# Performance work log

Measured on AMD Instinct MI355X. Metric: run time of the kernel, lower is better.

The kernel has to match this reference:

```python
import jax, jax.numpy as jnp
import numpy as np
import math

B, L, D, H = 2, 2048, 1024, 16
DK = D // H

def setup_inputs() -> dict:
    key = jax.random.key(0)
    ks = jax.random.split(key, 12)
    s = 1.0 / math.sqrt(D)
    inp = {
        "Q": jax.random.normal(ks[0], (B, L, D), jnp.float32),
        "K": jax.random.normal(ks[1], (B, L, D), jnp.float32),
        "V": jax.random.normal(ks[2], (B, L, D), jnp.float32),
        "mask": jnp.tril(jnp.ones((L, L), jnp.bool_))[None, None],  # [1,1,L,L] causal
        "Wq_w": jax.random.normal(ks[3], (D, D), jnp.float32) * s,
        "Wq_b": jnp.zeros((D,), jnp.float32),
        "Wk_w": jax.random.normal(ks[4], (D, D), jnp.float32) * s,
        "Wk_b": jnp.zeros((D,), jnp.float32),
        "Wv_w": jax.random.normal(ks[5], (D, D), jnp.float32) * s,
        "Wv_b": jnp.zeros((D,), jnp.float32),
        "fc_w": jax.random.normal(ks[6], (D, D), jnp.float32) * s,
        "fc_b": jnp.zeros((D,), jnp.float32),
    }
    return inp

def reference(Q, K, V, mask, Wq_w, Wq_b, Wk_w, Wk_b, Wv_w, Wv_b, fc_w, fc_b):
    # torch Linear: y = x @ W.T + b
    def split_heads(x):
        return x.reshape(B, L, H, DK).transpose(0, 2, 1, 3)  # [B,H,L,DK]
    q = split_heads(Q @ Wq_w.T + Wq_b)
    k = split_heads(K @ Wk_w.T + Wk_b)
    v = split_heads(V @ Wv_w.T + Wv_b)
    scores = jnp.einsum("bhqd,bhkd->bhqk", q, k) / math.sqrt(DK)
    scores = jnp.where(mask, scores, jnp.float32(-1e9))
    attn = jax.nn.softmax(scores, axis=-1)
    out = jnp.einsum("bhqk,bhkd->bhqd", attn, v)
    out = out.transpose(0, 2, 1, 3).reshape(B, L, D)
    return out @ fc_w.T + fc_b
```

## Files before the change

kernel.cpp:

```cpp
#include <hip/hip_runtime.h>
#include <hip/hip_bf16.h>
#include <math.h>

typedef __attribute__((ext_vector_type(8))) short short8;
typedef __attribute__((ext_vector_type(4))) short short4v;
typedef __attribute__((ext_vector_type(4))) float float4v;
typedef __attribute__((ext_vector_type(2))) unsigned int uint2v;

static constexpr int Bc = 2, Lc = 2048, Dc = 1024, Hc = 16;
static constexpr float C1 = 0.125f * 1.44269504088896f;
static constexpr float C2 = -8.0f * 1.44269504088896f;

__device__ __forceinline__ short f2bf(float x) {
    unsigned int b = __float_as_uint(x);
    return (short)((b + 0x7FFFu + ((b >> 16) & 1u)) >> 16);
}

__device__ __forceinline__ void gld16(const void* g, void* l) {
    __builtin_amdgcn_global_load_lds(
        (const __attribute__((address_space(1))) unsigned int*)g,
        (__attribute__((address_space(3))) unsigned int*)l, 16, 0, 0);
}

__global__ __launch_bounds__(256) void cvt_all(
    const float* q, const float* k, const float* v,
    const float* wq, const float* wk, const float* wv, const float* fw,
    short* qo, short* ko, short* vo,
    short* wqo, short* wko, short* wvo, short* fwo)
{
    const int z = blockIdx.y;
    const float* s; short* d; int n;
    switch (z) {
        case 0: s = q;  d = qo;  n = Bc*Lc*Dc; break;
        case 1: s = k;  d = ko;  n = Bc*Lc*Dc; break;
        case 2: s = v;  d = vo;  n = Bc*Lc*Dc; break;
        case 3: s = wq; d = wqo; n = Dc*Dc; break;
        case 4: s = wk; d = wko; n = Dc*Dc; break;
        case 5: s = wv; d = wvo; n = Dc*Dc; break;
        default: s = fw; d = fwo; n = Dc*Dc; break;
    }
    const int idx = (blockIdx.x * 256 + threadIdx.x) * 8;
    if (idx >= n) return;
    float4 lo = *reinterpret_cast<const float4*>(s + idx);
    float4 hi = *reinterpret_cast<const float4*>(s + idx + 4);
    short8 o = short8{f2bf(lo.x), f2bf(lo.y), f2bf(lo.z), f2bf(lo.w),
                      f2bf(hi.x), f2bf(hi.y), f2bf(hi.z), f2bf(hi.w)};
    *reinterpret_cast<short8*>(d + idx) = o;
}

struct GemmCtx {
    int lane, w, wm, wn, quad, l16, bm0, bn0, srow, soct;
};
__device__ __forceinline__ void gemm_core(
    const short* __restrict__ A, const short* __restrict__ Bt,
    short* As, short* Bs, const GemmCtx& c, float4v acc[4][4])
{
    const int K = Dc;
    const int l7 = c.l16 & 7;
    for (int k0 = 0; k0 < K; k0 += 64) {
#pragma unroll
        for (int rep = 0; rep < 4; ++rep) {
            const int rb = (c.w * 4 + rep) * 8;
            const int goct = c.soct ^ c.srow;
            gld16(A  + (size_t)(c.bm0 + rb + c.srow) * K + k0 + goct * 8,
                  &As[rb * 64]);
            gld16(Bt + (size_t)(c.bn0 + rb + c.srow) * K + k0 + goct * 8,
                  &Bs[rb * 64]);
        }
        __syncthreads();
#pragma unroll
        for (int s = 0; s < 2; ++s) {
            const int roct = (s * 4 + c.quad) ^ l7;
            short8 af[4], bf[4];
#pragma unroll
            for (int i = 0; i < 4; ++i)
                af[i] = *reinterpret_cast<const short8*>(
                    &As[(c.wm * 64 + i * 16 + c.l16) * 64 + roct * 8]);
#pragma unroll
            for (int j = 0; j < 4; ++j)
                bf[j] = *reinterpret_cast<const short8*>(
                    &Bs[(c.wn * 64 + j * 16 + c.l16) * 64 + roct * 8]);
#pragma unroll
            for (int i = 0; i < 4; ++i)
#pragma unroll
                for (int j = 0; j < 4; ++j)
                    acc[i][j] = __builtin_amdgcn_mfma_f32_16x16x32_bf16(af[i], bf[j], acc[i][j], 0, 0, 0);
        }
        __syncthreads();
    }
}
__device__ __forceinline__ GemmCtx make_ctx(int bm0, int bn0) {
    GemmCtx c;
    const int tid = threadIdx.x;
    c.lane = tid & 63; c.w = tid >> 6;
    c.wm = c.w >> 1;   c.wn = c.w & 1;
    c.quad = c.lane >> 4; c.l16 = c.lane & 15;
    c.bm0 = bm0; c.bn0 = bn0;
    c.srow = c.lane >> 3; c.soct = c.lane & 7;
    return c;
}

__global__ __launch_bounds__(256, 2) void qkv_gemm(
    const short* __restrict__ Qb, const short* __restrict__ Kb, const short* __restrict__ Vb,
    const short* __restrict__ Wq, const short* __restrict__ Wk, const short* __restrict__ Wv,
    const float* __restrict__ bq, const float* __restrict__ bk, const float* __restrict__ bv,
    short* __restrict__ q_ws, short* __restrict__ k_ws, short* __restrict__ vT_ws)
{
    __shared__ short As[128 * 64];
    __shared__ short Bs[128 * 64];
    const int id  = blockIdx.x;
    const int xcd = id & 7;
    const int seq = id >> 3;
    const int x   = seq & 7;
    const int yy  = (seq >> 3) & 3;
    const int z   = seq >> 5;
    const int y   = xcd * 4 + yy;

    const short* A    = (z == 0) ? Qb : (z == 1) ? Kb : Vb;
    const short* Bt   = (z == 0) ? Wq : (z == 1) ? Wk : Wv;
    const float* bias = (z == 0) ? bq : (z == 1) ? bk : bv;

    GemmCtx c = make_ctx(y * 128, x * 128);
    float4v acc[4][4] = {};
    gemm_core(A, Bt, As, Bs, c, acc);

    if (z < 2) {
        short* C = (z == 0) ? q_ws : k_ws;
#pragma unroll
        for (int j = 0; j < 4; ++j) {
            const int col = c.bn0 + c.wn * 64 + j * 16 + c.l16;
            const float bv2 = bias[col];
#pragma unroll
            for (int i = 0; i < 4; ++i)
#pragma unroll
                for (int r = 0; r < 4; ++r) {
                    const int row = c.bm0 + c.wm * 64 + i * 16 + c.quad * 4 + r;
                    C[(size_t)row * Dc + col] = f2bf(acc[i][j][r] + bv2);
                }
        }
    } else {
#pragma unroll
        for (int j = 0; j < 4; ++j) {
            const int col = c.bn0 + c.wn * 64 + j * 16 + c.l16;
            const float bv2 = bias[col];
            const int hh = col >> 6, d = col & 63;
#pragma unroll
            for (int i = 0; i < 4; ++i) {
                const int row0 = c.bm0 + c.wm * 64 + i * 16 + c.quad * 4;
                const int bb = row0 >> 11, l = row0 & 2047;
                short4v o4;
#pragma unroll
                for (int r = 0; r < 4; ++r) o4[r] = f2bf(acc[i][j][r] + bv2);
                *reinterpret_cast<short4v*>(
                    &vT_ws[((size_t)((bb * 16 + hh) * 64 + d)) * Lc + l]) = o4;
            }
        }
    }
}

__global__ __launch_bounds__(256, 2) void out_gemm(
    const short* __restrict__ A, const short* __restrict__ Bt,
    const float* __restrict__ bias, float* __restrict__ C)
{
    __shared__ short As[128 * 64];
    __shared__ short Bs[128 * 64];
    const int id  = blockIdx.x;
    const int xcd = id & 7;
    const int seq = id >> 3;
    const int x   = seq & 7;
    const int yy  = seq >> 3;
    const int y   = xcd * 4 + yy;

    GemmCtx c = make_ctx(y * 128, x * 128);
    float4v acc[4][4] = {};
    gemm_core(A, Bt, As, Bs, c, acc);
#pragma unroll
    for (int j = 0; j < 4; ++j) {
        const int col = c.bn0 + c.wn * 64 + j * 16 + c.l16;
        const float bv2 = bias[col];
#pragma unroll
        for (int i = 0; i < 4; ++i)
#pragma unroll
            for (int r = 0; r < 4; ++r) {
                const int row = c.bm0 + c.wm * 64 + i * 16 + c.quad * 4 + r;
                C[(size_t)row * Dc + col] = acc[i][j][r] + bv2;
            }
    }
}

__global__ __launch_bounds__(256, 4) void attn_flash7(
    const short* __restrict__ q_ws,
    const short* __restrict__ k_ws,
    const short* __restrict__ vT_ws,
    short* __restrict__ o_ws)
{
    __shared__ short Ks[2][64 * 64];
    __shared__ short Vs[2][64 * 64];

    const int tid  = threadIdx.x;
    const int lane = tid & 63;
    const int w    = tid >> 6;
    const int quad = lane >> 4;
    const int l16  = lane & 15;
    const int l7   = l16 & 7;

    const int id = blockIdx.x;
    const int g  = id >> 8;
    const int s  = (id >> 5) & 7;
    const int bh = id & 31;
    const int qi = (g == 0) ? (31 - s) : (g == 1) ? (23 - s)
                 : (g == 2) ? s        : (8 + s);
    const int b  = bh >> 4, h = bh & 15;

    const int srow = lane >> 3;
    const int soct = lane & 7;
    const size_t khead  = (size_t)(b * Lc) * Dc + h * 64;
    const size_t vthead = (size_t)(bh * 64) * Lc;
    const int xoct0 = quad ^ l7;
    const int xoct1 = (4 + quad) ^ l7;

    const short onev = (l16 == 0) ? (short)0x3F80 : (short)0;
    const short4v vb4 = short4v{onev, onev, onev, onev};

    auto stage = [&](int tile, int buf) {
#pragma unroll
        for (int rep = 0; rep < 2; ++rep) {
            const int issue = w * 2 + rep;
            const int grow = issue * 8 + srow;
            const int goct = soct ^ (grow & 7);
            gld16(k_ws + khead + (size_t)(tile * 64 + grow) * Dc + goct * 8,
                  &Ks[buf][issue * 512]);
            gld16(vT_ws + vthead + (size_t)grow * Lc + tile * 64 + goct * 8,
                  &Vs[buf][issue * 512]);
        }
    };

    const int q0   = qi * 64;
    const int qw0  = q0 + w * 16;
    const int qrow = qw0 + l16;

    short8 qf[2];
    {
        const size_t base = ((size_t)(b * Lc + qw0 + l16)) * Dc + h * 64;
        qf[0] = *reinterpret_cast<const short8*>(&q_ws[base + quad * 8]);
        qf[1] = *reinterpret_cast<const short8*>(&q_ws[base + 32 + quad * 8]);
    }

    float4v o_acc[5] = {};

    stage(0, 0);

#pragma unroll 1
    for (int kb = 0; kb <= qi; ++kb) {
        const int cur = kb & 1;
        if (kb < qi) {
            stage(kb + 1, cur ^ 1);
            asm volatile("s_waitcnt vmcnt(4)" ::: "memory");
        } else {
            asm volatile("s_waitcnt vmcnt(0)" ::: "memory");
        }
        __builtin_amdgcn_s_barrier();
        asm volatile("" ::: "memory");

        const short* Kc = &Ks[cur][0];
        const short* Vc = &Vs[cur][0];

        if (kb < qi) {
#pragma unroll
            for (int t = 0; t < 4; ++t) {
                short8 kf0 = *reinterpret_cast<const short8*>(&Kc[(t * 16 + l16) * 64 + xoct0 * 8]);
                short8 kf1 = *reinterpret_cast<const short8*>(&Kc[(t * 16 + l16) * 64 + xoct1 * 8]);
                float4v sv = {};
                sv = __builtin_amdgcn_mfma_f32_16x16x32_bf16(kf0, qf[0], sv, 0, 0, 0);
                sv = __builtin_amdgcn_mfma_f32_16x16x32_bf16(kf1, qf[1], sv, 0, 0, 0);

                short4v vb[4];
#pragma unroll
                for (int dt = 0; dt < 4; ++dt)
                    vb[dt] = *reinterpret_cast<const short4v*>(
                        &Vc[(dt * 16 + l16) * 64 + ((2 * t + (quad >> 1)) ^ l7) * 8 + (quad & 1) * 4]);

                unsigned u[4];
#pragma unroll
                for (int r = 0; r < 4; ++r)
                    u[r] = __float_as_uint(exp2f(fmaf(sv[r], C1, C2)));
                const uint2v pu = {__builtin_amdgcn_perm(u[1], u[0], 0x07060302u),
                                   __builtin_amdgcn_perm(u[3], u[2], 0x07060302u)};
                const short4v pa = __builtin_bit_cast(short4v, pu);

#pragma unroll
                for (int dt = 0; dt < 4; ++dt)
                    o_acc[dt] = __builtin_amdgcn_mfma_f32_16x16x16bf16_1k(pa, vb[dt], o_acc[dt], 0, 0, 0);
                o_acc[4] = __builtin_amdgcn_mfma_f32_16x16x16bf16_1k(pa, vb4, o_acc[4], 0, 0, 0);
            }
        } else {
#pragma unroll
            for (int t = 0; t < 4; ++t) {
                if (t <= w) {
                    short8 kf0 = *reinterpret_cast<const short8*>(&Kc[(t * 16 + l16) * 64 + xoct0 * 8]);
                    short8 kf1 = *reinterpret_cast<const short8*>(&Kc[(t * 16 + l16) * 64 + xoct1 * 8]);
                    float4v sv = {};
                    sv = __builtin_amdgcn_mfma_f32_16x16x32_bf16(kf0, qf[0], sv, 0, 0, 0);
                    sv = __builtin_amdgcn_mfma_f32_16x16x32_bf16(kf1, qf[1], sv, 0, 0, 0);

                    short4v vb[4];
#pragma unroll
                    for (int dt = 0; dt < 4; ++dt)
                        vb[dt] = *reinterpret_cast<const short4v*>(
                            &Vc[(dt * 16 + l16) * 64 + ((2 * t + (quad >> 1)) ^ l7) * 8 + (quad & 1) * 4]);

                    const int kbase = kb * 64 + t * 16 + quad * 4;
                    unsigned u[4];
                    if (t < w) {
#pragma unroll
                        for (int r = 0; r < 4; ++r)
                            u[r] = __float_as_uint(exp2f(fmaf(sv[r], C1, C2)));
                    } else {
#pragma unroll
                        for (int r = 0; r < 4; ++r) {
                            const float pv = (kbase + r <= qrow)
                                           ? exp2f(fmaf(sv[r], C1, C2)) : 0.f;
                            u[r] = __float_as_uint(pv);
                        }
                    }
                    const uint2v pu = {__builtin_amdgcn_perm(u[1], u[0], 0x07060302u),
                                       __builtin_amdgcn_perm(u[3], u[2], 0x07060302u)};
                    const short4v pa = __builtin_bit_cast(short4v, pu);

#pragma unroll
                    for (int dt = 0; dt < 4; ++dt)
                        o_acc[dt] = __builtin_amdgcn_mfma_f32_16x16x16bf16_1k(pa, vb[dt], o_acc[dt], 0, 0, 0);
                    o_acc[4] = __builtin_amdgcn_mfma_f32_16x16x16bf16_1k(pa, vb4, o_acc[4], 0, 0, 0);
                }
            }
        }
        asm volatile("" ::: "memory");
        __builtin_amdgcn_s_barrier();
    }

#pragma unroll
    for (int r = 0; r < 4; ++r) {
        const float lsum = __shfl(o_acc[4][r], quad << 4, 64);
        const float inv = 1.f / lsum;
        const int qr = qw0 + quad * 4 + r;
#pragma unroll
        for (int dt = 0; dt < 4; ++dt)
            o_ws[((size_t)(b * Lc + qr)) * Dc + h * 64 + dt * 16 + l16] =
                f2bf(o_acc[dt][r] * inv);
    }
}

extern "C" void kernel_launch(void* const* d_in, const int* in_sizes, int n_in,
                              void* d_out, int out_size, void* d_ws, size_t ws_size,
                              hipStream_t stream)
{
    const float* Q = (const float*)d_in[0];
    const float* K = (const float*)d_in[1];
    const float* V = (const float*)d_in[2];

    int w0 = -1;
    for (int i = 3; i + 8 <= n_in; ++i) {
        bool ok = true;
        for (int j = 0; j < 4 && ok; ++j)
            ok = (in_sizes[i + 2 * j] == Dc * Dc) && (in_sizes[i + 2 * j + 1] == Dc);
        if (ok) { w0 = i; break; }
    }
    if (w0 < 0) w0 = (n_in >= 12) ? 4 : 3;

    const float* Wq_w = (const float*)d_in[w0 + 0];
    const float* Wq_b = (const float*)d_in[w0 + 1];
    const float* Wk_w = (const float*)d_in[w0 + 2];
    const float* Wk_b = (const float*)d_in[w0 + 3];
    const float* Wv_w = (const float*)d_in[w0 + 4];
    const float* Wv_b = (const float*)d_in[w0 + 5];
    const float* fc_w = (const float*)d_in[w0 + 6];
    const float* fc_b = (const float*)d_in[w0 + 7];
    float* out = (float*)d_out;

    const size_t nel = (size_t)Bc * Lc * Dc;
    const size_t nw  = (size_t)Dc * Dc;
    short* p = (short*)d_ws;
    short* xq   = p;  p += nel;
    short* xk   = p;  p += nel;
    short* xv   = p;  p += nel;
    short* wqb  = p;  p += nw;
    short* wkb  = p;  p += nw;
    short* wvb  = p;  p += nw;
    short* fwb  = p;  p += nw;
    short* q_ws = p;  p += nel;
    short* k_ws = p;  p += nel;
    short* vT_ws= p;  p += nel;
    short* a_ws = xq;

    cvt_all<<<dim3(2048, 7), 256, 0, stream>>>(
        Q, K, V, Wq_w, Wk_w, Wv_w, fc_w, xq, xk, xv, wqb, wkb, wvb, fwb);

    qkv_gemm<<<dim3(768), 256, 0, stream>>>(
        xq, xk, xv, wqb, wkb, wvb, Wq_b, Wk_b, Wv_b, q_ws, k_ws, vT_ws);

    attn_flash7<<<dim3(1024), 256, 0, stream>>>(q_ws, k_ws, vT_ws, a_ws);

    out_gemm<<<dim3(256), 256, 0, stream>>>(a_ws, fwb, fc_b, out);
}
```

Baseline: 223.5 us.

## Split attention KV loop across two warp groups per block and combine partials

Attention blocks now use 512 threads as two groups of four waves. Each group handles alternating key tiles (even or odd) of the causal range with its own double-buffered LDS region. The unnormalised partial outputs and row sums are merged through shared memory before normalisation. The block schedule also becomes a simple largest-first order in place of the interleaved mapping. This halves the serial KV loop per block to shorten the critical path of long rows, at the cost of doubled LDS per block (64KB), lower possible occupancy, and an extra combine step.

```diff
diff --git a/kernel.cpp b/kernel.cpp
--- a/kernel.cpp
+++ b/kernel.cpp
@@ -188,28 +188,26 @@
     }
 }
 
-__global__ __launch_bounds__(256, 4) void attn_flash7(
+__global__ __launch_bounds__(512, 4) void attn_flash12(
     const short* __restrict__ q_ws,
     const short* __restrict__ k_ws,
     const short* __restrict__ vT_ws,
     short* __restrict__ o_ws)
 {
-    __shared__ short Ks[2][64 * 64];
-    __shared__ short Vs[2][64 * 64];
+    __shared__ __align__(16) short KV[2][2][2][64 * 64];
 
     const int tid  = threadIdx.x;
     const int lane = tid & 63;
-    const int w    = tid >> 6;
+    const int w8   = tid >> 6;
+    const int grp  = w8 >> 2;
+    const int wq   = w8 & 3;
     const int quad = lane >> 4;
     const int l16  = lane & 15;
     const int l7   = l16 & 7;
 
     const int id = blockIdx.x;
-    const int g  = id >> 8;
-    const int s  = (id >> 5) & 7;
+    const int qi = 31 - (id >> 5);
     const int bh = id & 31;
-    const int qi = (g == 0) ? (31 - s) : (g == 1) ? (23 - s)
-                 : (g == 2) ? s        : (8 + s);
     const int b  = bh >> 4, h = bh & 15;
 
     const int srow = lane >> 3;
@@ -222,21 +220,24 @@
     const short onev = (l16 == 0) ? (short)0x3F80 : (short)0;
     const short4v vb4 = short4v{onev, onev, onev, onev};
 
+    const int cnt = (grp <= qi) ? (((qi - grp) >> 1) + 1) : 0;
+    const int nit = (qi >> 1) + 1;
+
     auto stage = [&](int tile, int buf) {
 #pragma unroll
         for (int rep = 0; rep < 2; ++rep) {
-            const int issue = w * 2 + rep;
+            const int issue = wq * 2 + rep;
             const int grow = issue * 8 + srow;
             const int goct = soct ^ (grow & 7);
             gld16(k_ws + khead + (size_t)(tile * 64 + grow) * Dc + goct * 8,
-                  &Ks[buf][issue * 512]);
+                  &KV[grp][buf][0][issue * 512]);
             gld16(vT_ws + vthead + (size_t)grow * Lc + tile * 64 + goct * 8,
-                  &Vs[buf][issue * 512]);
+                  &KV[grp][buf][1][issue * 512]);
         }
     };
 
     const int q0   = qi * 64;
-    const int qw0  = q0 + w * 16;
+    const int qw0  = q0 + wq * 16;
     const int qrow = qw0 + l16;
 
     short8 qf[2];
@@ -248,13 +249,13 @@
 
     float4v o_acc[5] = {};
 
-    stage(0, 0);
+    if (cnt > 0) stage(grp, 0);
 
 #pragma unroll 1
-    for (int kb = 0; kb <= qi; ++kb) {
-        const int cur = kb & 1;
-        if (kb < qi) {
-            stage(kb + 1, cur ^ 1);
+    for (int si = 0; si < nit; ++si) {
+        const int cur = si & 1;
+        if (si + 1 < cnt) {
+            stage(2 * (si + 1) + grp, cur ^ 1);
             asm volatile("s_waitcnt vmcnt(4)" ::: "memory");
         } else {
             asm volatile("s_waitcnt vmcnt(0)" ::: "memory");
@@ -262,41 +263,14 @@
         __builtin_amdgcn_s_barrier();
         asm volatile("" ::: "memory");
 
-        const short* Kc = &Ks[cur][0];
-        const short* Vc = &Vs[cur][0];
-
-        if (kb < qi) {
-#pragma unroll
-            for (int t = 0; t < 4; ++t) {
-                short8 kf0 = *reinterpret_cast<const short8*>(&Kc[(t * 16 + l16) * 64 + xoct0 * 8]);
-                short8 kf1 = *reinterpret_cast<const short8*>(&Kc[(t * 16 + l16) * 64 + xoct1 * 8]);
-                float4v sv = {};
-                sv = __builtin_amdgcn_mfma_f32_16x16x32_bf16(kf0, qf[0], sv, 0, 0, 0);
-                sv = __builtin_amdgcn_mfma_f32_16x16x32_bf16(kf1, qf[1], sv, 0, 0, 0);
-
-                short4v vb[4];
-#pragma unroll
-                for (int dt = 0; dt < 4; ++dt)
-                    vb[dt] = *reinterpret_cast<const short4v*>(
-                        &Vc[(dt * 16 + l16) * 64 + ((2 * t + (quad >> 1)) ^ l7) * 8 + (quad & 1) * 4]);
-
-                unsigned u[4];
-#pragma unroll
-                for (int r = 0; r < 4; ++r)
-                    u[r] = __float_as_uint(exp2f(fmaf(sv[r], C1, C2)));
-                const uint2v pu = {__builtin_amdgcn_perm(u[1], u[0], 0x07060302u),
-                                   __builtin_amdgcn_perm(u[3], u[2], 0x07060302u)};
-                const short4v pa = __builtin_bit_cast(short4v, pu);
-
-#pragma unroll
-                for (int dt = 0; dt < 4; ++dt)
-                    o_acc[dt] = __builtin_amdgcn_mfma_f32_16x16x16bf16_1k(pa, vb[dt], o_acc[dt], 0, 0, 0);
-                o_acc[4] = __builtin_amdgcn_mfma_f32_16x16x16bf16_1k(pa, vb4, o_acc[4], 0, 0, 0);
-            }
-        } else {
-#pragma unroll
-            for (int t = 0; t < 4; ++t) {
-                if (t <= w) {
+        if (si < cnt) {
+            const int kb = 2 * si + grp;
+            const short* Kc = &KV[grp][cur][0][0];
+            const short* Vc = &KV[grp][cur][1][0];
+
+            if (kb < qi) {
+#pragma unroll
+                for (int t = 0; t < 4; ++t) {
                     short8 kf0 = *reinterpret_cast<const short8*>(&Kc[(t * 16 + l16) * 64 + xoct0 * 8]);
                     short8 kf1 = *reinterpret_cast<const short8*>(&Kc[(t * 16 + l16) * 64 + xoct1 * 8]);
                     float4v sv = {};
@@ -309,20 +283,10 @@
                         vb[dt] = *reinterpret_cast<const short4v*>(
                             &Vc[(dt * 16 + l16) * 64 + ((2 * t + (quad >> 1)) ^ l7) * 8 + (quad & 1) * 4]);
 
-                    const int kbase = kb * 64 + t * 16 + quad * 4;
                     unsigned u[4];
-                    if (t < w) {
-#pragma unroll
-                        for (int r = 0; r < 4; ++r)
-                            u[r] = __float_as_uint(exp2f(fmaf(sv[r], C1, C2)));
-                    } else {
-#pragma unroll
-                        for (int r = 0; r < 4; ++r) {
-                            const float pv = (kbase + r <= qrow)
-                                           ? exp2f(fmaf(sv[r], C1, C2)) : 0.f;
-                            u[r] = __float_as_uint(pv);
-                        }
-                    }
+#pragma unroll
+                    for (int r = 0; r < 4; ++r)
+                        u[r] = __float_as_uint(exp2f(fmaf(sv[r], C1, C2)));
                     const uint2v pu = {__builtin_amdgcn_perm(u[1], u[0], 0x07060302u),
                                        __builtin_amdgcn_perm(u[3], u[2], 0x07060302u)};
                     const short4v pa = __builtin_bit_cast(short4v, pu);
@@ -332,21 +296,74 @@
                         o_acc[dt] = __builtin_amdgcn_mfma_f32_16x16x16bf16_1k(pa, vb[dt], o_acc[dt], 0, 0, 0);
                     o_acc[4] = __builtin_amdgcn_mfma_f32_16x16x16bf16_1k(pa, vb4, o_acc[4], 0, 0, 0);
                 }
+            } else {
+#pragma unroll
+                for (int t = 0; t < 4; ++t) {
+                    if (t <= wq) {
+                        short8 kf0 = *reinterpret_cast<const short8*>(&Kc[(t * 16 + l16) * 64 + xoct0 * 8]);
+                        short8 kf1 = *reinterpret_cast<const short8*>(&Kc[(t * 16 + l16) * 64 + xoct1 * 8]);
+                        float4v sv = {};
+                        sv = __builtin_amdgcn_mfma_f32_16x16x32_bf16(kf0, qf[0], sv, 0, 0, 0);
+                        sv = __builtin_amdgcn_mfma_f32_16x16x32_bf16(kf1, qf[1], sv, 0, 0, 0);
+
+                        short4v vb[4];
+#pragma unroll
+                        for (int dt = 0; dt < 4; ++dt)
+                            vb[dt] = *reinterpret_cast<const short4v*>(
+                                &Vc[(dt * 16 + l16) * 64 + ((2 * t + (quad >> 1)) ^ l7) * 8 + (quad & 1) * 4]);
+
+                        const int kbase = kb * 64 + t * 16 + quad * 4;
+                        unsigned u[4];
+                        if (t < wq) {
+#pragma unroll
+                            for (int r = 0; r < 4; ++r)
+                                u[r] = __float_as_uint(exp2f(fmaf(sv[r], C1, C2)));
+                        } else {
+#pragma unroll
+                            for (int r = 0; r < 4; ++r) {
+                                const float pv = (kbase + r <= qrow)
+                                               ? exp2f(fmaf(sv[r], C1, C2)) : 0.f;
+                                u[r] = __float_as_uint(pv);
+                            }
+                        }
+                        const uint2v pu = {__builtin_amdgcn_perm(u[1], u[0], 0x07060302u),
+                                           __builtin_amdgcn_perm(u[3], u[2], 0x07060302u)};
+                        const short4v pa = __builtin_bit_cast(short4v, pu);
+
+#pragma unroll
+                        for (int dt = 0; dt < 4; ++dt)
+                            o_acc[dt] = __builtin_amdgcn_mfma_f32_16x16x16bf16_1k(pa, vb[dt], o_acc[dt], 0, 0, 0);
+                        o_acc[4] = __builtin_amdgcn_mfma_f32_16x16x16bf16_1k(pa, vb4, o_acc[4], 0, 0, 0);
+                    }
+                }
             }
         }
         asm volatile("" ::: "memory");
         __builtin_amdgcn_s_barrier();
     }
 
-#pragma unroll
-    for (int r = 0; r < 4; ++r) {
-        const float lsum = __shfl(o_acc[4][r], quad << 4, 64);
-        const float inv = 1.f / lsum;
-        const int qr = qw0 + quad * 4 + r;
-#pragma unroll
-        for (int dt = 0; dt < 4; ++dt)
-            o_ws[((size_t)(b * Lc + qr)) * Dc + h * 64 + dt * 16 + l16] =
-                f2bf(o_acc[dt][r] * inv);
+    __syncthreads();
+    float4v* cmb = reinterpret_cast<float4v*>(&KV[0][0][0][0]);
+    if (grp == 1) {
+#pragma unroll
+        for (int dt = 0; dt < 5; ++dt)
+            cmb[dt * 256 + wq * 64 + lane] = o_acc[dt];
+    }
+    __syncthreads();
+    if (grp == 0) {
+#pragma unroll
+        for (int dt = 0; dt < 5; ++dt)
+            o_acc[dt] += cmb[dt * 256 + wq * 64 + lane];
+#pragma unroll
+        for (int r = 0; r < 4; ++r) {
+            const float lsum = __shfl(o_acc[4][r], quad << 4, 64);
+            const float inv = 1.f / lsum;
+            const int qr = qw0 + quad * 4 + r;
+#pragma unroll
+            for (int dt = 0; dt < 4; ++dt)
+                o_ws[((size_t)(b * Lc + qr)) * Dc + h * 64 + dt * 16 + l16] =
+                    f2bf(o_acc[dt][r] * inv);
+        }
     }
 }
 
@@ -398,7 +415,7 @@
     qkv_gemm<<<dim3(768), 256, 0, stream>>>(
         xq, xk, xv, wqb, wkb, wvb, Wq_b, Wk_b, Wv_b, q_ws, k_ws, vT_ws);
 
-    attn_flash7<<<dim3(1024), 256, 0, stream>>>(q_ws, k_ws, vT_ws, a_ws);
+    attn_flash12<<<dim3(1024), 512, 0, stream>>>(q_ws, k_ws, vT_ws, a_ws);
 
     out_gemm<<<dim3(256), 256, 0, stream>>>(a_ws, fwb, fc_b, out);
 }
```

After: 217.2 us. 2.8% less time.
